# Kernel tuning notes

Measured on AMD Instinct MI355X. Metric: run time of the kernel, lower is better.

## Reference

```python
import jax, jax.numpy as jnp
import numpy as np

NUM_CLASSES = 21
THRESH = 0.5
NEG_POS = 3
VAR0, VAR1 = 0.1, 0.2


def point_form(boxes):
    # center form (cx,cy,w,h) -> corner form (x1,y1,x2,y2)
    return jnp.concatenate([boxes[:, :2] - boxes[:, 2:] / 2,
                            boxes[:, :2] + boxes[:, 2:] / 2], axis=1)


def jaccard(a, b):
    # a: [N,4] corner form, b: [P,4] corner form -> IoU [N,P]
    lt = jnp.maximum(a[:, None, :2], b[None, :, :2])
    rb = jnp.minimum(a[:, None, 2:], b[None, :, 2:])
    wh = jnp.clip(rb - lt, 0.0)
    inter = wh[..., 0] * wh[..., 1]
    area_a = (a[:, 2] - a[:, 0]) * (a[:, 3] - a[:, 1])
    area_b = (b[:, 2] - b[:, 0]) * (b[:, 3] - b[:, 1])
    return inter / (area_a[:, None] + area_b[None, :] - inter)


def match_one(truths, labels, priors):
    # truths: [N,4] corner form, labels: [N] int, priors: [P,4] center form
    ov = jaccard(truths, point_form(priors))            # [N,P]
    best_prior_idx = jnp.argmax(ov, axis=1)             # [N] best prior per truth
    best_truth_ov = jnp.max(ov, axis=0)                 # [P]
    best_truth_idx = jnp.argmax(ov, axis=0)             # [P]
    # ensure each truth keeps its best prior
    best_truth_ov = best_truth_ov.at[best_prior_idx].set(2.0)
    best_truth_idx = best_truth_idx.at[best_prior_idx].set(
        jnp.arange(truths.shape[0], dtype=best_truth_idx.dtype))
    matches = truths[best_truth_idx]                    # [P,4]
    conf = labels[best_truth_idx] + 1                   # [P]
    conf = jnp.where(best_truth_ov < THRESH, 0, conf)
    # encode
    g_cxcy = ((matches[:, :2] + matches[:, 2:]) / 2 - priors[:, :2]) / (VAR0 * priors[:, 2:])
    g_wh = jnp.log((matches[:, 2:] - matches[:, :2]) / priors[:, 2:]) / VAR1
    return jnp.concatenate([g_cxcy, g_wh], axis=1), conf


def setup_inputs() -> dict:
    key = jax.random.key(0)
    k1, k2, k3, k4, k5, k6, k7 = jax.random.split(key, 7)
    B, P, C, N = 64, 24564, NUM_CLASSES, 16
    loc_data = jax.random.normal(k1, (B, P, 4), dtype=jnp.float32)
    conf_data = jax.random.normal(k2, (B, P, C), dtype=jnp.float32)
    # priors: valid center-form boxes
    ctr = 0.05 + 0.9 * jax.random.uniform(k3, (P, 2), dtype=jnp.float32)
    pwh = 0.05 + 0.25 * jax.random.uniform(k4, (P, 2), dtype=jnp.float32)
    priors = jnp.concatenate([ctr, pwh], axis=1)
    # truths: valid corner-form boxes
    xy1 = 0.7 * jax.random.uniform(k5, (B, N, 2), dtype=jnp.float32)
    twh = 0.05 + 0.2 * jax.random.uniform(k6, (B, N, 2), dtype=jnp.float32)
    truths = jnp.concatenate([xy1, xy1 + twh], axis=2)
    labels = jax.random.randint(k7, (B, N), 0, 20, dtype=jnp.int32)
    return {"loc_data": loc_data, "conf_data": conf_data, "priors": priors,
            "truths": truths, "labels": labels}


def reference(loc_data, conf_data, priors, truths, labels):
    B, P, C = conf_data.shape
    loc_t, conf_t = jax.vmap(lambda t, l: match_one(t, l, priors))(truths, labels)
    pos = conf_t > 0                                     # [B,P]

    # localization smooth-L1, summed over positives
    diff = loc_data - loc_t
    ad = jnp.abs(diff)
    sl1 = jnp.where(ad < 1.0, 0.5 * diff * diff, ad - 0.5)
    loss_l = jnp.sum(sl1 * pos[..., None].astype(loc_data.dtype))

    # per-prior CE = logsumexp - logit at matched class
    lse = jax.nn.logsumexp(conf_data, axis=2)            # [B,P]
    gathered = jnp.take_along_axis(conf_data, conf_t[..., None].astype(jnp.int32), axis=2)[..., 0]
    loss_c_all = lse - gathered

    # hard-negative mining via double argsort rank (pos zeroed first)
    loss_c_mine = jnp.where(pos, 0.0, loss_c_all)
    idx_rank = jnp.argsort(jnp.argsort(-loss_c_mine, axis=1), axis=1)
    num_pos = jnp.sum(pos, axis=1, keepdims=True)        # [B,1]
    num_neg = jnp.minimum(NEG_POS * num_pos, P - 1)
    neg = idx_rank < num_neg

    mask = pos | neg
    loss_c = jnp.sum(jnp.where(mask, loss_c_all, 0.0))

    n = jnp.sum(num_pos).astype(loc_data.dtype)
    return loss_l / n, loss_c / n
```

## Files before the change

kernel.cpp:

```cpp
#include <hip/hip_runtime.h>
#include <cstdint>
#include <cstddef>

#define B_ 64
#define P_ 24564
#define C_ 21
#define N_ 16
#define NPB_ 24
#define THRESH_ 0.5f


__device__ inline unsigned long long shfl_down_u64(unsigned long long v, int off) {
    unsigned lo = (unsigned)v, hi = (unsigned)(v >> 32);
    lo = __shfl_down(lo, off);
    hi = __shfl_down(hi, off);
    return ((unsigned long long)hi << 32) | lo;
}

__device__ inline float sl1_encode(float4 ld, float4 pr,
                                   float tx1, float ty1, float tx2, float ty2) {
    float gcx = ((tx1 + tx2) * 0.5f - pr.x) / (0.1f * pr.z);
    float gcy = ((ty1 + ty2) * 0.5f - pr.y) / (0.1f * pr.w);
    float gw  = __logf((tx2 - tx1) / pr.z) / 0.2f;
    float gh  = __logf((ty2 - ty1) / pr.w) / 0.2f;
    float g[4] = {gcx, gcy, gw, gh};
    float l[4] = {ld.x, ld.y, ld.z, ld.w};
    float s = 0.0f;
#pragma unroll
    for (int i = 0; i < 4; i++) {
        float d = l[i] - g[i];
        float ad = fabsf(d);
        s += (ad < 1.0f) ? 0.5f * d * d : ad - 0.5f;
    }
    return s;
}


__global__ __launch_bounds__(256, 4) void
kA_fused(const float* __restrict__ loc,
         const float* __restrict__ conf,
         const float* __restrict__ priors,
         const float* __restrict__ truths,
         const int* __restrict__ labels,
         float* __restrict__ mine,
         float* __restrict__ part_ll,
         float* __restrict__ part_pce,
         int* __restrict__ part_np,
         unsigned long long* __restrict__ part_key) {
    int b = blockIdx.y, bx = blockIdx.x, t = threadIdx.x;
    int wid = t >> 6, lane = t & 63;
    __shared__ float tr[N_ * 4];
    __shared__ int lb[N_];
    __shared__ unsigned skey[N_ * 256];
    __shared__ float sll[4], spc[4];
    __shared__ int snp[4];
    if (t < N_ * 4) tr[t] = truths[b * N_ * 4 + t];
    if (t < N_) lb[t] = labels[b * N_ + t];
    __syncthreads();

    int p0 = bx * 1024 + 4 * t;
    bool valid = p0 < P_;

    float px1[4], py1[4], px2[4], py2[4], ap[4];
#pragma unroll
    for (int r = 0; r < 4; r++) {
        float4 pr = valid ? ((const float4*)priors)[p0 + r]
                          : make_float4(0.5f, 0.5f, 0.1f, 0.1f);
        px1[r] = pr.x - pr.z * 0.5f; py1[r] = pr.y - pr.w * 0.5f;
        px2[r] = pr.x + pr.z * 0.5f; py2[r] = pr.y + pr.w * 0.5f;
        ap[r] = (px2[r] - px1[r]) * (py2[r] - py1[r]);
    }

    float best[4] = {-1.0f, -1.0f, -1.0f, -1.0f};
    int bn[4] = {0, 0, 0, 0};
#pragma unroll
    for (int n = 0; n < N_; n++) {
        float tx1 = tr[n * 4 + 0], ty1 = tr[n * 4 + 1];
        float tx2 = tr[n * 4 + 2], ty2 = tr[n * 4 + 3];
        float at = (tx2 - tx1) * (ty2 - ty1);
        float tbi = -1.0f;
        int tbr = 0;
#pragma unroll
        for (int r = 0; r < 4; r++) {
            float lx = fmaxf(tx1, px1[r]), ly = fmaxf(ty1, py1[r]);
            float rx = fminf(tx2, px2[r]), ry = fminf(ty2, py2[r]);
            float w = fmaxf(rx - lx, 0.0f), h = fmaxf(ry - ly, 0.0f);
            float inter = w * h;
            float iou = inter / (at + ap[r] - inter);
            if (iou > best[r]) { best[r] = iou; bn[r] = n; }
            if (iou > tbi) { tbi = iou; tbr = r; }
        }
        skey[n * 256 + t] = valid
            ? ((__float_as_uint(tbi) << 2) | (unsigned)(3 - tbr)) : 0u;
    }

    int bti[4], pos[4];
    float g[4];
    const float* cbase = conf + ((size_t)b * P_ + p0) * C_;
#pragma unroll
    for (int r = 0; r < 4; r++) {
        bti[r] = bn[r];
        pos[r] = (best[r] < THRESH_) ? 0 : 1;
        int cls = pos[r] ? (lb[bti[r]] + 1) : 0;
        g[r] = valid ? cbase[r * C_ + cls] : 0.0f;
    }

    __syncthreads();
#pragma unroll
    for (int i = 0; i < 4; i++) {
        int n = wid + 4 * i;
        unsigned long long bk = 0ull;
#pragma unroll
        for (int q = 0; q < 4; q++) {
            int tt = lane + 64 * q;
            unsigned k32 = skey[n * 256 + tt];
            unsigned long long v = ((unsigned long long)k32 << 32) |
                                   (unsigned)~(unsigned)tt;
            bk = (v > bk) ? v : bk;
        }
        for (int off = 32; off; off >>= 1) {
            unsigned long long o = shfl_down_u64(bk, off);
            bk = (o > bk) ? o : bk;
        }
        if (lane == 0) {
            int twin = (int)~(unsigned)(bk & 0xFFFFFFFFull);
            unsigned k32 = (unsigned)(bk >> 32);
            int pwin = bx * 1024 + 4 * twin + (3 - (int)(k32 & 3u));
            part_key[(size_t)(b * NPB_ + bx) * N_ + n] =
                ((unsigned long long)(k32 >> 2) << 32) | (unsigned)~(unsigned)pwin;
        }
    }

    float s[4] = {0.0f, 0.0f, 0.0f, 0.0f};
    if (valid) {
        const float4* src = (const float4*)(conf + ((size_t)b * P_ + (size_t)bx * 1024) * C_)
                            + (size_t)t * 21;
#pragma unroll
        for (int i = 0; i < 21; i++) {
            float4 v = src[i];
            s[(4 * i + 0) / 21] += __expf(v.x);
            s[(4 * i + 1) / 21] += __expf(v.y);
            s[(4 * i + 2) / 21] += __expf(v.z);
            s[(4 * i + 3) / 21] += __expf(v.w);
        }
    }

    float ll = 0.0f, pce = 0.0f;
    int np = 0;
    if (valid) {
        float mv[4];
#pragma unroll
        for (int r = 0; r < 4; r++) {
            float lca = fmaxf(__logf(s[r]) - g[r], 0.0f);
            mv[r] = pos[r] ? 0.0f : lca;
            if (pos[r]) {
                np++;
                pce += lca;
                float4 prr = ((const float4*)priors)[p0 + r];
                float4 ld = ((const float4*)loc)[(size_t)b * P_ + p0 + r];
                ll += sl1_encode(ld, prr, tr[bti[r] * 4 + 0], tr[bti[r] * 4 + 1],
                                 tr[bti[r] * 4 + 2], tr[bti[r] * 4 + 3]);
            }
        }
        *(float4*)(mine + (size_t)b * P_ + p0) = make_float4(mv[0], mv[1], mv[2], mv[3]);
    }

    for (int off = 32; off; off >>= 1) {
        ll += __shfl_down(ll, off);
        pce += __shfl_down(pce, off);
        np += __shfl_down(np, off);
    }
    if (lane == 0) { sll[wid] = ll; spc[wid] = pce; snp[wid] = np; }
    __syncthreads();
    if (t == 0) {
        float a = 0.0f, cc = 0.0f;
        int q = 0;
        for (int i = 0; i < 4; i++) { a += sll[i]; cc += spc[i]; q += snp[i]; }
        part_ll[b * NPB_ + bx] = a;
        part_pce[b * NPB_ + bx] = cc;
        part_np[b * NPB_ + bx] = q;
    }
}

__global__ __launch_bounds__(1024) void
kB_batch(const float* __restrict__ loc,
         const float* __restrict__ conf,
         const float* __restrict__ priors,
         const float* __restrict__ truths,
         const int* __restrict__ labels,
         const float* __restrict__ mine,
         const float* __restrict__ part_ll,
         const float* __restrict__ part_pce,
         const int* __restrict__ part_np,
         const unsigned long long* __restrict__ part_key,
         double* __restrict__ bll,
         double* __restrict__ bpc,
         int* __restrict__ bnp) {
    int b = blockIdx.x, t = threadIdx.x, wid = t >> 6, lane = t & 63;
    __shared__ float tr[N_ * 4];
    __shared__ int lb[N_];
    __shared__ int sp[N_];
    __shared__ float sdll, sdpce, sll_s, spc_s;
    __shared__ int sdnp, snp_s;
    __shared__ int scnt[16];
    __shared__ unsigned sT;
    __shared__ float wsum[16];
    __shared__ int wcgt[16];

    if (t < N_ * 4) tr[t] = truths[b * N_ * 4 + t];
    if (t < N_) lb[t] = labels[b * N_ + t];
    if (t == 0) { sdll = 0.f; sdpce = 0.f; sdnp = 0; sll_s = 0.f; spc_s = 0.f; snp_s = 0; }
    if (t < N_) {
        unsigned long long best = 0ull;
        for (int i = 0; i < NPB_; i++) {
            unsigned long long k = part_key[(size_t)(b * NPB_ + i) * N_ + t];
            best = (k > best) ? k : best;
        }
        sp[t] = (int)~(unsigned)(best & 0xFFFFFFFFull);
    }
    __syncthreads();
    if (t < NPB_) {
        atomicAdd(&sll_s, part_ll[b * NPB_ + t]);
        atomicAdd(&spc_s, part_pce[b * NPB_ + t]);
        atomicAdd(&snp_s, part_np[b * NPB_ + t]);
    }
    if (t < N_) {
        int p = sp[t];
        bool last = true;
        for (int n = t + 1; n < N_; n++) if (sp[n] == p) last = false;
        if (last) {
            int nf = t;
            float4 pr = ((const float4*)priors)[p];
            float px1 = pr.x - pr.z * 0.5f, py1 = pr.y - pr.w * 0.5f;
            float px2 = pr.x + pr.z * 0.5f, py2 = pr.y + pr.w * 0.5f;
            float ap = (px2 - px1) * (py2 - py1);
            float best = -1.0f;
            int bti = 0;
            for (int n = 0; n < N_; n++) {
                float tx1 = tr[n * 4], ty1 = tr[n * 4 + 1];
                float tx2 = tr[n * 4 + 2], ty2 = tr[n * 4 + 3];
                float at = (tx2 - tx1) * (ty2 - ty1);
                float lx = fmaxf(tx1, px1), ly = fmaxf(ty1, py1);
                float rx = fminf(tx2, px2), ry = fminf(ty2, py2);
                float w = fmaxf(rx - lx, 0.0f), h = fmaxf(ry - ly, 0.0f);
                float inter = w * h;
                float iou = inter / (at + ap - inter);
                if (iou > best) { best = iou; bti = n; }
            }
            int pos_old = (best >= THRESH_) ? 1 : 0;
            const float* cp = conf + ((size_t)b * P_ + p) * C_;
            float x[C_];
            float ssum = 0.0f;
            for (int j = 0; j < C_; j++) { x[j] = cp[j]; ssum += __expf(x[j]); }
            float lse = __logf(ssum);
            float4 ld = ((const float4*)loc)[(size_t)b * P_ + p];
            float dll = sl1_encode(ld, pr, tr[nf * 4], tr[nf * 4 + 1],
                                   tr[nf * 4 + 2], tr[nf * 4 + 3]);
            float dpce = lse - x[lb[nf] + 1];
            int dnp = 1 - pos_old;
            if (pos_old) {
                dll -= sl1_encode(ld, pr, tr[bti * 4], tr[bti * 4 + 1],
                                  tr[bti * 4 + 2], tr[bti * 4 + 3]);
                dpce -= lse - x[lb[bti] + 1];
            }
            atomicAdd(&sdll, dll);
            atomicAdd(&sdpce, dpce);
            atomicAdd(&sdnp, dnp);
        }
    }

    unsigned omask = 0;
#pragma unroll
    for (int n = 0; n < N_; n++) {
        int p = sp[n];
        if ((p & 1023) == t) omask |= 1u << (p >> 10);
    }
    const float* v = mine + (size_t)b * P_;
    int nel = (t < (P_ - 23 * 1024)) ? 24 : 23;
    float xv[24];
#pragma unroll
    for (int i = 0; i < 24; i++) {
        float x = 0.0f;
        if (i < nel) x = v[t + (i << 10)];
        if ((omask >> i) & 1) x = 0.0f;
        xv[i] = x;
    }
    __syncthreads();
    int np = snp_s + sdnp;
    int k = np * 3;
    if (k > P_ - 1) k = P_ - 1;

    unsigned T = 0u;
    for (int bpos = 30; bpos >= 0; bpos--) {
        unsigned cand = T | (1u << bpos);
        int c = 0;
#pragma unroll
        for (int i = 0; i < 24; i++)
            if (__float_as_uint(xv[i]) >= cand) c++;
        for (int off = 32; off; off >>= 1) c += __shfl_down(c, off);
        if (lane == 0) scnt[wid] = c;
        __syncthreads();
        if (t == 0) {
            int tot = 0;
            for (int i = 0; i < 16; i++) tot += scnt[i];
            sT = (tot >= k) ? cand : T;
        }
        __syncthreads();
        T = sT;
    }

    float psum = 0.0f;
    int cgt = 0;
#pragma unroll
    for (int i = 0; i < 24; i++) {
        if (__float_as_uint(xv[i]) > T) { psum += xv[i]; cgt++; }
    }
    for (int off = 32; off; off >>= 1) {
        psum += __shfl_down(psum, off);
        cgt += __shfl_down(cgt, off);
    }
    if (lane == 0) { wsum[wid] = psum; wcgt[wid] = cgt; }
    __syncthreads();
    if (t == 0) {
        float s2 = 0.0f;
        int cg = 0;
        for (int i = 0; i < 16; i++) { s2 += wsum[i]; cg += wcgt[i]; }
        int skrem = k - cg;
        double tot = (double)s2 + (double)skrem * (double)__uint_as_float(T);
        bll[b] = (double)(sll_s + sdll);
        bpc[b] = (double)(spc_s + sdpce) + tot;
        bnp[b] = np;
    }
}

__global__ void kC_final(const double* __restrict__ bll,
                         const double* __restrict__ bpc,
                         const int* __restrict__ bnp,
                         float* __restrict__ out) {
    int t = threadIdx.x;
    double a = bll[t], c = bpc[t];
    int n = bnp[t];
    for (int off = 32; off; off >>= 1) {
        a += __shfl_down(a, off);
        c += __shfl_down(c, off);
        n += __shfl_down(n, off);
    }
    if (t == 0) {
        double dn = (double)n;
        out[0] = (float)(a / dn);
        out[1] = (float)(c / dn);
    }
}


extern "C" void kernel_launch(void* const* d_in, const int* in_sizes, int n_in,
                              void* d_out, int out_size, void* d_ws, size_t ws_size,
                              hipStream_t stream) {
    const float* loc    = (const float*)d_in[0];
    const float* conf   = (const float*)d_in[1];
    const float* priors = (const float*)d_in[2];
    const float* truths = (const float*)d_in[3];
    const int*   labels = (const int*)d_in[4];
    float* out = (float*)d_out;

    char* ws = (char*)d_ws;
    unsigned long long* part_key = (unsigned long long*)(ws);
    float*  part_ll  = (float*)(ws + 196608);
    float*  part_pce = (float*)(ws + 202752);
    int*    part_np  = (int*)(ws + 208896);
    double* bll      = (double*)(ws + 215040);
    double* bpc      = (double*)(ws + 215552);
    int*    bnp      = (int*)(ws + 216064);
    float*  mine     = (float*)(ws + 262144);

    hipLaunchKernelGGL(kA_fused, dim3(NPB_, B_), dim3(256), 0, stream,
                       loc, conf, priors, truths, labels,
                       mine, part_ll, part_pce, part_np, part_key);
    hipLaunchKernelGGL(kB_batch, dim3(B_), dim3(1024), 0, stream,
                       loc, conf, priors, truths, labels, mine,
                       part_ll, part_pce, part_np, part_key, bll, bpc, bnp);
    hipLaunchKernelGGL(kC_final, dim3(1), dim3(64), 0, stream, bll, bpc, bnp, out);
}
```

Measured before the change: 271.4 us.

## Split fused match/LSE kernel into separate match and logsumexp kernels

Splits the fused first kernel into a matching kernel and a separate logsumexp/loss kernel. The matching kernel writes each prior's best-truth index and positive flag as a packed byte to a workspace buffer, and the LSE kernel reads it back. The aim is to lower register and shared-memory pressure in each kernel so the conf-streaming pass gets better occupancy and latency hiding. In exchange it adds a kernel launch, an extra global round trip for the packed match words, and reads the truths a second time.

```diff
diff --git a/kernel.cpp b/kernel.cpp
--- a/kernel.cpp
+++ b/kernel.cpp
@@ -37,25 +37,15 @@
 
 
 __global__ __launch_bounds__(256, 4) void
-kA_fused(const float* __restrict__ loc,
-         const float* __restrict__ conf,
-         const float* __restrict__ priors,
+kM_match(const float* __restrict__ priors,
          const float* __restrict__ truths,
-         const int* __restrict__ labels,
-         float* __restrict__ mine,
-         float* __restrict__ part_ll,
-         float* __restrict__ part_pce,
-         int* __restrict__ part_np,
+         uint32_t* __restrict__ matchw,
          unsigned long long* __restrict__ part_key) {
     int b = blockIdx.y, bx = blockIdx.x, t = threadIdx.x;
     int wid = t >> 6, lane = t & 63;
     __shared__ float tr[N_ * 4];
-    __shared__ int lb[N_];
     __shared__ unsigned skey[N_ * 256];
-    __shared__ float sll[4], spc[4];
-    __shared__ int snp[4];
     if (t < N_ * 4) tr[t] = truths[b * N_ * 4 + t];
-    if (t < N_) lb[t] = labels[b * N_ + t];
     __syncthreads();
 
     int p0 = bx * 1024 + 4 * t;
@@ -94,15 +84,14 @@
             ? ((__float_as_uint(tbi) << 2) | (unsigned)(3 - tbr)) : 0u;
     }
 
-    int bti[4], pos[4];
-    float g[4];
-    const float* cbase = conf + ((size_t)b * P_ + p0) * C_;
-#pragma unroll
-    for (int r = 0; r < 4; r++) {
-        bti[r] = bn[r];
-        pos[r] = (best[r] < THRESH_) ? 0 : 1;
-        int cls = pos[r] ? (lb[bti[r]] + 1) : 0;
-        g[r] = valid ? cbase[r * C_ + cls] : 0.0f;
+    if (valid) {
+        uint32_t w = 0;
+#pragma unroll
+        for (int r = 0; r < 4; r++) {
+            uint32_t byte = (uint32_t)bn[r] | ((best[r] < THRESH_) ? 0u : 0x10u);
+            w |= byte << (8 * r);
+        }
+        matchw[(size_t)b * (P_ / 4) + (p0 >> 2)] = w;
     }
 
     __syncthreads();
@@ -130,11 +119,48 @@
                 ((unsigned long long)(k32 >> 2) << 32) | (unsigned)~(unsigned)pwin;
         }
     }
+}
+
+__global__ __launch_bounds__(256, 4) void
+kL_lse(const float* __restrict__ loc,
+       const float* __restrict__ conf,
+       const float* __restrict__ priors,
+       const float* __restrict__ truths,
+       const int* __restrict__ labels,
+       const uint32_t* __restrict__ matchw,
+       float* __restrict__ mine,
+       float* __restrict__ part_ll,
+       float* __restrict__ part_pce,
+       int* __restrict__ part_np) {
+    int b = blockIdx.y, bx = blockIdx.x, t = threadIdx.x;
+    int wid = t >> 6, lane = t & 63;
+    __shared__ float tr[N_ * 4];
+    __shared__ int lb[N_];
+    __shared__ float sll[4], spc[4];
+    __shared__ int snp[4];
+    if (t < N_ * 4) tr[t] = truths[b * N_ * 4 + t];
+    if (t < N_) lb[t] = labels[b * N_ + t];
+    __syncthreads();
+
+    int p0 = bx * 1024 + 4 * t;
+    bool valid = p0 < P_;
+
+    uint32_t mw = valid ? matchw[(size_t)b * (P_ / 4) + (p0 >> 2)] : 0u;
+    int bti[4], pos[4];
+    float g[4];
+    const float* cbase = conf + ((size_t)b * P_ + p0) * C_;
+#pragma unroll
+    for (int r = 0; r < 4; r++) {
+        uint32_t byte = (mw >> (8 * r)) & 0xFFu;
+        bti[r] = (int)(byte & 15u);
+        pos[r] = (int)(byte >> 4);
+        int cls = pos[r] ? (lb[bti[r]] + 1) : 0;
+        g[r] = valid ? cbase[r * C_ + cls] : 0.0f;
+    }
 
     float s[4] = {0.0f, 0.0f, 0.0f, 0.0f};
     if (valid) {
-        const float4* src = (const float4*)(conf + ((size_t)b * P_ + (size_t)bx * 1024) * C_)
-                            + (size_t)t * 21;
+        const float4* src = (const float4*)cbase;
 #pragma unroll
         for (int i = 0; i < 21; i++) {
             float4 v = src[i];
@@ -372,10 +398,13 @@
     double* bpc      = (double*)(ws + 215552);
     int*    bnp      = (int*)(ws + 216064);
     float*  mine     = (float*)(ws + 262144);
-
-    hipLaunchKernelGGL(kA_fused, dim3(NPB_, B_), dim3(256), 0, stream,
-                       loc, conf, priors, truths, labels,
-                       mine, part_ll, part_pce, part_np, part_key);
+    uint32_t* matchw = (uint32_t*)(ws + 6553600);
+
+    hipLaunchKernelGGL(kM_match, dim3(NPB_, B_), dim3(256), 0, stream,
+                       priors, truths, matchw, part_key);
+    hipLaunchKernelGGL(kL_lse, dim3(NPB_, B_), dim3(256), 0, stream,
+                       loc, conf, priors, truths, labels, matchw,
+                       mine, part_ll, part_pce, part_np);
     hipLaunchKernelGGL(kB_batch, dim3(B_), dim3(1024), 0, stream,
                        loc, conf, priors, truths, labels, mine,
                        part_ll, part_pce, part_np, part_key, bll, bpc, bnp);
```

New measurement: 293.5 us. +8.1%, slower.
